# Performance work log

Hardware: AMD Instinct MI355X
Metric: run time of the kernel (lower is better)

## Reference

```python
import jax, jax.numpy as jnp
import numpy as np

B, N, D, H = 16, 1024, 768, 12
HD = D // H
SCALE = HD ** -0.5


def setup_inputs() -> dict:
    key = jax.random.key(0)
    ks = jax.random.split(key, 7)
    s = D ** -0.5
    return {
        "x": jax.random.normal(ks[0], (B, N, D), dtype=jnp.float32),
        "Wq": jax.random.normal(ks[1], (D, D), dtype=jnp.float32) * s,
        "bq": jax.random.normal(ks[2], (D,), dtype=jnp.float32) * 0.01,
        "Wk": jax.random.normal(ks[3], (D, D), dtype=jnp.float32) * s,
        "bk": jax.random.normal(ks[4], (D,), dtype=jnp.float32) * 0.01,
        "Wv": jax.random.normal(ks[5], (D, D), dtype=jnp.float32) * s,
        "bv": jax.random.normal(ks[6], (D,), dtype=jnp.float32) * 0.01,
    }


def _split_heads(t):
    # [B, N, D] -> [B, H, N, HD]
    return t.reshape(B, N, H, HD).transpose(0, 2, 1, 3)


def reference(x, Wq, bq, Wk, bk, Wv, bv):
    q = _split_heads(x @ Wq + bq)
    k = _split_heads(x @ Wk + bk)
    v = _split_heads(x @ Wv + bv)
    # [B, H, N, N] attention scores, fp32 softmax (matches eager path)
    scores = jnp.einsum("bhqd,bhkd->bhqk", q, k) * SCALE
    attn = jax.nn.softmax(scores.astype(jnp.float32), axis=-1).astype(q.dtype)
    # dropout p=0 in eval mode -> identity
    ctx = jnp.einsum("bhqk,bhkd->bhqd", attn, v)  # [B, H, N, HD]
    ctx = ctx.transpose(0, 2, 1, 3).reshape(B, N, D)
    return ctx
```

## Files before the change

kernel.cpp:

```cpp
#include <hip/hip_runtime.h>

#define B_ 16
#define N_ 1024
#define D_ 768
#define H_ 12
#define HD_ 64
#define QSCALE 0.18033688011112042f

typedef __attribute__((ext_vector_type(8))) __bf16 bf16x8;
typedef __attribute__((ext_vector_type(4))) float f32x4;
typedef unsigned short u16;
typedef unsigned int u32;

__device__ inline u16 f2bf(float f) {
    u32 u = __builtin_bit_cast(u32, f);
    u += 0x7fffu + ((u >> 16) & 1u);
    return (u16)(u >> 16);
}

__device__ inline float fexp2(float x) {
#if __has_builtin(__builtin_amdgcn_exp2f)
    return __builtin_amdgcn_exp2f(x);
#else
    return exp2f(x);
#endif
}

__device__ inline u32 cvt_pk_bf16(float a, float b) {
    u32 r;
    asm("v_cvt_pk_bf16_f32 %0, %1, %2" : "=v"(r) : "v"(a), "v"(b));
    return r;
}

__device__ inline void gl_lds16(const u16* gp, u16* lp_) {
    __builtin_amdgcn_global_load_lds(
        (const __attribute__((address_space(1))) u32*)(gp),
        (__attribute__((address_space(3))) u32*)(lp_), 16, 0, 0);
}

__global__ __launch_bounds__(256) void prep_kernel(
    const float* __restrict__ x, u16* __restrict__ xbf,
    const float* __restrict__ Wq, const float* __restrict__ Wk,
    const float* __restrict__ Wv, u16* __restrict__ wtall) {
    const int bid = blockIdx.x, tid = threadIdx.x;
    if (bid < 6144) {
        int i = bid * 256 + tid;
        const float4* p = (const float4*)x;
        float4 a = p[2 * i], b = p[2 * i + 1];
        union { u16 us[8]; int4 v; } u;
        u.us[0] = f2bf(a.x); u.us[1] = f2bf(a.y); u.us[2] = f2bf(a.z); u.us[3] = f2bf(a.w);
        u.us[4] = f2bf(b.x); u.us[5] = f2bf(b.y); u.us[6] = f2bf(b.z); u.us[7] = f2bf(b.w);
        ((int4*)xbf)[i] = u.v;
    } else {
        __shared__ u16 t[32][33];
        int wb = bid - 6144;
        int z = wb / 576, rem = wb % 576;
        int bx = rem % 24, by = rem / 24;
        const float* W = z == 0 ? Wq : (z == 1 ? Wk : Wv);
        u16* Wt = wtall + (size_t)z * D_ * D_;
        int n0 = bx * 32, k0 = by * 32;
        int tx = tid & 31, ty = tid >> 5;
#pragma unroll
        for (int i = 0; i < 4; i++) {
            int k = k0 + ty + i * 8;
            t[ty + i * 8][tx] = f2bf(W[k * D_ + n0 + tx]);
        }
        __syncthreads();
#pragma unroll
        for (int i = 0; i < 4; i++) {
            int n = n0 + ty + i * 8;
            Wt[n * D_ + k0 + tx] = t[tx][ty + i * 8];
        }
    }
}

__global__ __launch_bounds__(256) void qkv2_kernel(
    const u16* __restrict__ xbf, const u16* __restrict__ wtall,
    const float* __restrict__ bq, const float* __restrict__ bk, const float* __restrict__ bv,
    u16* __restrict__ qbf, u16* __restrict__ kbf, u16* __restrict__ vtbf) {
    __shared__ u16 lsA[2][128 * 64];
    __shared__ u16 lsB[2][128 * 64];

    const int mt = blockIdx.x, nt = blockIdx.y;
    const int tid = threadIdx.x, w = tid >> 6, lane = tid & 63;
    const int g = lane >> 4, c = lane & 15;
    const int wr = w >> 1, wc = w & 1;
    const int m0 = mt * 128, n0 = nt * 128;

    const u16* pa[4];
    const u16* pb[4];
#pragma unroll
    for (int i = 0; i < 4; i++) {
        int ch = (i * 4 + w) * 64 + lane;
        int row = ch >> 3, c8 = ch & 7;
        pa[i] = xbf + (size_t)(m0 + row) * D_ + c8 * 8;
        pb[i] = wtall + (size_t)(n0 + row) * D_ + c8 * 8;
    }

#define STAGE(bi, koff) do {                                       \
        _Pragma("unroll")                                          \
        for (int i = 0; i < 4; i++) {                              \
            gl_lds16(pa[i] + (koff), &lsA[bi][(i * 4 + w) * 512]); \
            gl_lds16(pb[i] + (koff), &lsB[bi][(i * 4 + w) * 512]); \
        }                                                          \
    } while (0)

    f32x4 acc[4][4];
#pragma unroll
    for (int i = 0; i < 4; i++)
#pragma unroll
        for (int j = 0; j < 4; j++) acc[i][j] = (f32x4){0.f, 0.f, 0.f, 0.f};

    STAGE(0, 0);
    __syncthreads();
    int cur = 0;

    for (int kt = 0; kt < 12; kt++) {
        if (kt < 11) STAGE(cur ^ 1, (kt + 1) * 64);
#pragma unroll
        for (int kk = 0; kk < 2; kk++) {
            bf16x8 af[4], bfr[4];
#pragma unroll
            for (int f = 0; f < 4; f++)
                af[f] = *(const bf16x8*)&lsA[cur][(wr * 64 + f * 16 + c) * 64 + kk * 32 + g * 8];
#pragma unroll
            for (int f = 0; f < 4; f++)
                bfr[f] = *(const bf16x8*)&lsB[cur][(wc * 64 + f * 16 + c) * 64 + kk * 32 + g * 8];
#pragma unroll
            for (int fr = 0; fr < 4; fr++)
#pragma unroll
                for (int fc = 0; fc < 4; fc++)
                    acc[fr][fc] = __builtin_amdgcn_mfma_f32_16x16x32_bf16(
                        af[fr], bfr[fc], acc[fr][fc], 0, 0, 0);
        }
        __syncthreads();
        cur ^= 1;
    }
#undef STAGE

    const int mode = nt / 6;
    const int ncol0 = (nt % 6) * 128;
    const float* bias = mode == 0 ? bq : (mode == 1 ? bk : bv);
    float bb[4];
#pragma unroll
    for (int fc = 0; fc < 4; fc++) bb[fc] = bias[ncol0 + wc * 64 + fc * 16 + c];

    if (mode < 2) {
        u16* outp = mode == 0 ? qbf : kbf;
        const float osc = mode == 0 ? QSCALE : 1.0f;
#pragma unroll
        for (int fc = 0; fc < 4; fc++) {
            int col = ncol0 + wc * 64 + fc * 16 + c;
            int head = col >> 6, hd = col & 63;
#pragma unroll
            for (int fr = 0; fr < 4; fr++)
#pragma unroll
                for (int rr = 0; rr < 4; rr++) {
                    int m = m0 + wr * 64 + fr * 16 + g * 4 + rr;
                    int b = m >> 10, nn = m & 1023;
                    outp[(((size_t)b * H_ + head) * N_ + nn) * HD_ + hd] =
                        f2bf((acc[fr][fc][rr] + bb[fc]) * osc);
                }
        }
    } else {
#pragma unroll
        for (int fc = 0; fc < 4; fc++) {
            int col = ncol0 + wc * 64 + fc * 16 + c;
            int head = col >> 6, hd = col & 63;
#pragma unroll
            for (int fr = 0; fr < 4; fr++) {
                int m = m0 + wr * 64 + fr * 16 + g * 4;
                int b = m >> 10, nn = m & 1023;
                union { u16 us[4]; int2 v; } u;
#pragma unroll
                for (int rr = 0; rr < 4; rr++) u.us[rr] = f2bf(acc[fr][fc][rr] + bb[fc]);
                *(int2*)&vtbf[(((size_t)b * H_ + head) * HD_ + hd) * N_ + nn] = u.v;
            }
        }
    }
}

__global__ __launch_bounds__(256) void attn_kernel(
    const u16* __restrict__ qbf, const u16* __restrict__ kbf,
    const u16* __restrict__ vtbf, float* __restrict__ out) {
    __shared__ u16 lk[2][64][72];
    __shared__ u16 lv[2][64][72];

    const int bh = blockIdx.x;
    const int qt = blockIdx.y;
    const int b = bh / H_, h = bh % H_;
    const int tid = threadIdx.x;
    const int w = tid >> 6, lane = tid & 63, g = lane >> 4, c = lane & 15;
    const int q0 = qt * 128;

    bf16x8 aq[2][2];
#pragma unroll
    for (int ss = 0; ss < 2; ss++) {
        const u16* qr = qbf + ((size_t)bh * N_ + q0 + w * 32 + ss * 16 + c) * HD_;
        aq[ss][0] = *(const bf16x8*)&qr[g * 8];
        aq[ss][1] = *(const bf16x8*)&qr[32 + g * 8];
    }

    const u16* kbase = kbf + (size_t)bh * N_ * HD_;
    const u16* vbase = vtbf + (size_t)bh * HD_ * N_;
    const int r0 = tid >> 3, c80 = (tid & 7) * 8;
    const int r1 = r0 + 32;

    int4 kreg0, kreg1, vreg0, vreg1;
#define LOADT(KV) do { \
        kreg0 = *(const int4*)(kbase + (size_t)((KV) + r0) * HD_ + c80); \
        kreg1 = *(const int4*)(kbase + (size_t)((KV) + r1) * HD_ + c80); \
        vreg0 = *(const int4*)(vbase + (size_t)r0 * N_ + (KV) + c80); \
        vreg1 = *(const int4*)(vbase + (size_t)r1 * N_ + (KV) + c80); \
    } while (0)
#define WRITET(bi) do { \
        *(int4*)&lk[bi][r0][c80] = kreg0; \
        *(int4*)&lk[bi][r1][c80] = kreg1; \
        *(int4*)&lv[bi][r0][c80] = vreg0; \
        *(int4*)&lv[bi][r1][c80] = vreg1; \
    } while (0)

    const f32x4 zf = (f32x4){0.f, 0.f, 0.f, 0.f};
    f32x4 o[2][4];
#pragma unroll
    for (int ss = 0; ss < 2; ss++)
#pragma unroll
        for (int i = 0; i < 4; i++) o[ss][i] = zf;
    float lr[2] = {0.f, 0.f};

    LOADT(0);
    WRITET(0);
    __syncthreads();
    int cur = 0;

    for (int kv0 = 0; kv0 < N_; kv0 += 64) {
        const bool more = (kv0 + 64) < N_;
        if (more) LOADT(kv0 + 64);

        f32x4 sc[2][4];
#pragma unroll
        for (int nf = 0; nf < 4; nf++) {
            bf16x8 ak0 = *(const bf16x8*)&lk[cur][nf * 16 + c][g * 8];
            bf16x8 ak1 = *(const bf16x8*)&lk[cur][nf * 16 + c][32 + g * 8];
            __builtin_amdgcn_s_setprio(1);
#pragma unroll
            for (int ss = 0; ss < 2; ss++) {
                sc[ss][nf] = __builtin_amdgcn_mfma_f32_16x16x32_bf16(ak0, aq[ss][0], zf, 0, 0, 0);
                sc[ss][nf] = __builtin_amdgcn_mfma_f32_16x16x32_bf16(ak1, aq[ss][1], sc[ss][nf], 0, 0, 0);
            }
            __builtin_amdgcn_s_setprio(0);
        }

        u32 pkk[2][4][2];
#pragma unroll
        for (int ss = 0; ss < 2; ss++) {
            f32x4 rsv = zf;
#pragma unroll
            for (int nf = 0; nf < 4; nf++) {
#pragma unroll
                for (int r = 0; r < 4; r++) sc[ss][nf][r] = fexp2(sc[ss][nf][r]);
                rsv += sc[ss][nf];
                pkk[ss][nf][0] = cvt_pk_bf16(sc[ss][nf][0], sc[ss][nf][1]);
                pkk[ss][nf][1] = cvt_pk_bf16(sc[ss][nf][2], sc[ss][nf][3]);
            }
            lr[ss] += (rsv[0] + rsv[1]) + (rsv[2] + rsv[3]);
        }

        bf16x8 pa[2][2];
#pragma unroll
        for (int ss = 0; ss < 2; ss++) {
            union { u32 ui[4]; bf16x8 v; } u0, u1;
            u0.ui[0] = pkk[ss][0][0]; u0.ui[1] = pkk[ss][0][1];
            u0.ui[2] = pkk[ss][1][0]; u0.ui[3] = pkk[ss][1][1];
            u1.ui[0] = pkk[ss][2][0]; u1.ui[1] = pkk[ss][2][1];
            u1.ui[2] = pkk[ss][3][0]; u1.ui[3] = pkk[ss][3][1];
            pa[ss][0] = u0.v; pa[ss][1] = u1.v;
        }

#pragma unroll
        for (int nf = 0; nf < 4; nf++) {
            union { int2 d[2]; bf16x8 v; } b0, b1;
            b0.d[0] = *(const int2*)&lv[cur][nf * 16 + c][4 * g];
            b0.d[1] = *(const int2*)&lv[cur][nf * 16 + c][16 + 4 * g];
            b1.d[0] = *(const int2*)&lv[cur][nf * 16 + c][32 + 4 * g];
            b1.d[1] = *(const int2*)&lv[cur][nf * 16 + c][48 + 4 * g];
            __builtin_amdgcn_s_setprio(1);
#pragma unroll
            for (int ss = 0; ss < 2; ss++) {
                o[ss][nf] = __builtin_amdgcn_mfma_f32_16x16x32_bf16(pa[ss][0], b0.v, o[ss][nf], 0, 0, 0);
                o[ss][nf] = __builtin_amdgcn_mfma_f32_16x16x32_bf16(pa[ss][1], b1.v, o[ss][nf], 0, 0, 0);
            }
            __builtin_amdgcn_s_setprio(0);
        }

        if (more) WRITET(cur ^ 1);
        __syncthreads();
        cur ^= 1;
    }
#undef LOADT
#undef WRITET

#pragma unroll
    for (int ss = 0; ss < 2; ss++) {
        float lf = lr[ss];
        lf += __shfl_xor(lf, 16);
        lf += __shfl_xor(lf, 32);
        float lq[4];
#pragma unroll
        for (int r = 0; r < 4; r++) lq[r] = __shfl(lf, g * 4 + r);
#pragma unroll
        for (int r = 0; r < 4; r++) {
            float inv = 1.f / lq[r];
            int n = q0 + w * 32 + ss * 16 + g * 4 + r;
#pragma unroll
            for (int nf = 0; nf < 4; nf++)
                out[((size_t)(b * N_ + n)) * D_ + h * HD_ + nf * 16 + c] = o[ss][nf][r] * inv;
        }
    }
}

extern "C" void kernel_launch(void* const* d_in, const int* in_sizes, int n_in,
                              void* d_out, int out_size, void* d_ws, size_t ws_size,
                              hipStream_t stream) {
    const float* x  = (const float*)d_in[0];
    const float* Wq = (const float*)d_in[1];
    const float* bq = (const float*)d_in[2];
    const float* Wk = (const float*)d_in[3];
    const float* bk = (const float*)d_in[4];
    const float* Wv = (const float*)d_in[5];
    const float* bv = (const float*)d_in[6];
    float* out = (float*)d_out;

    char* ws = (char*)d_ws;
    u16* xbf   = (u16*)ws;
    u16* wtall = (u16*)(ws + 25165824);
    u16* qbf   = (u16*)(ws + 28704768);
    u16* kbf   = (u16*)(ws + 53870592);
    u16* vtbf  = (u16*)(ws + 79036416);

    prep_kernel<<<7872, 256, 0, stream>>>(x, xbf, Wq, Wk, Wv, wtall);
    dim3 gg(128, 18);
    qkv2_kernel<<<gg, 256, 0, stream>>>(xbf, wtall, bq, bk, bv, qbf, kbf, vtbf);
    dim3 ga(192, 8);
    attn_kernel<<<ga, 256, 0, stream>>>(qbf, kbf, vtbf, out);
}
```

Baseline: 174.8 us.

## Pipeline QKV GEMM loads with 4-slot LDS ring and vmcnt waits

Restructures the QKV projection GEMM main loop from a double-buffered 64-wide K stage into a 4-slot ring of 32-wide K slices with two slices prefetched ahead. It replaces full __syncthreads with explicit s_waitcnt vmcnt counters plus a raw s_barrier, so global-to-LDS copies stay in flight across compute steps. The goal is to hide more global load latency behind MFMA work. LDS use stays the same. The risks are the hand-counted vmcnt values and the ring reuse: a barrier placed only before compute may leave a write-after-read hazard on a slot that is being refilled.

After: 175.5 us. No clear change (+0.4%).

```diff
diff --git a/kernel.cpp b/kernel.cpp
--- a/kernel.cpp
+++ b/kernel.cpp
@@ -78,8 +78,8 @@
     const u16* __restrict__ xbf, const u16* __restrict__ wtall,
     const float* __restrict__ bq, const float* __restrict__ bk, const float* __restrict__ bv,
     u16* __restrict__ qbf, u16* __restrict__ kbf, u16* __restrict__ vtbf) {
-    __shared__ u16 lsA[2][128 * 64];
-    __shared__ u16 lsB[2][128 * 64];
+    __shared__ u16 lsA[4 * 4096];
+    __shared__ u16 lsB[4 * 4096];
 
     const int mt = blockIdx.x, nt = blockIdx.y;
     const int tid = threadIdx.x, w = tid >> 6, lane = tid & 63;
@@ -87,22 +87,17 @@
     const int wr = w >> 1, wc = w & 1;
     const int m0 = mt * 128, n0 = nt * 128;
 
-    const u16* pa[4];
-    const u16* pb[4];
-#pragma unroll
-    for (int i = 0; i < 4; i++) {
-        int ch = (i * 4 + w) * 64 + lane;
-        int row = ch >> 3, c8 = ch & 7;
-        pa[i] = xbf + (size_t)(m0 + row) * D_ + c8 * 8;
-        pb[i] = wtall + (size_t)(n0 + row) * D_ + c8 * 8;
-    }
-
-#define STAGE(bi, koff) do {                                       \
-        _Pragma("unroll")                                          \
-        for (int i = 0; i < 4; i++) {                              \
-            gl_lds16(pa[i] + (koff), &lsA[bi][(i * 4 + w) * 512]); \
-            gl_lds16(pb[i] + (koff), &lsB[bi][(i * 4 + w) * 512]); \
-        }                                                          \
+    const int row0 = tid >> 2, cp0 = tid & 3;
+    const u16* ba0 = xbf + (size_t)(m0 + row0) * D_ + cp0 * 8;
+    const u16* ba1 = xbf + (size_t)(m0 + row0 + 64) * D_ + cp0 * 8;
+    const u16* bb0 = wtall + (size_t)(n0 + row0) * D_ + cp0 * 8;
+    const u16* bb1 = wtall + (size_t)(n0 + row0 + 64) * D_ + cp0 * 8;
+
+#define STAGEP(slot, p) do {                                   \
+        gl_lds16(ba0 + (p) * 32, &lsA[(slot) * 4096 + w * 512]);        \
+        gl_lds16(ba1 + (p) * 32, &lsA[(slot) * 4096 + 2048 + w * 512]); \
+        gl_lds16(bb0 + (p) * 32, &lsB[(slot) * 4096 + w * 512]);        \
+        gl_lds16(bb1 + (p) * 32, &lsB[(slot) * 4096 + 2048 + w * 512]); \
     } while (0)
 
     f32x4 acc[4][4];
@@ -111,32 +106,41 @@
 #pragma unroll
         for (int j = 0; j < 4; j++) acc[i][j] = (f32x4){0.f, 0.f, 0.f, 0.f};
 
-    STAGE(0, 0);
-    __syncthreads();
-    int cur = 0;
-
-    for (int kt = 0; kt < 12; kt++) {
-        if (kt < 11) STAGE(cur ^ 1, (kt + 1) * 64);
-#pragma unroll
-        for (int kk = 0; kk < 2; kk++) {
-            bf16x8 af[4], bfr[4];
-#pragma unroll
-            for (int f = 0; f < 4; f++)
-                af[f] = *(const bf16x8*)&lsA[cur][(wr * 64 + f * 16 + c) * 64 + kk * 32 + g * 8];
-#pragma unroll
-            for (int f = 0; f < 4; f++)
-                bfr[f] = *(const bf16x8*)&lsB[cur][(wc * 64 + f * 16 + c) * 64 + kk * 32 + g * 8];
-#pragma unroll
-            for (int fr = 0; fr < 4; fr++)
-#pragma unroll
-                for (int fc = 0; fc < 4; fc++)
-                    acc[fr][fc] = __builtin_amdgcn_mfma_f32_16x16x32_bf16(
-                        af[fr], bfr[fc], acc[fr][fc], 0, 0, 0);
-        }
-        __syncthreads();
-        cur ^= 1;
-    }
-#undef STAGE
+#define COMPUTE(s) do {                                                         \
+        bf16x8 af[4], bfr[4];                                                   \
+        _Pragma("unroll")                                                       \
+        for (int f = 0; f < 4; f++)                                             \
+            af[f] = *(const bf16x8*)&lsA[(s) * 4096 + (wr * 64 + f * 16 + c) * 32 + g * 8]; \
+        _Pragma("unroll")                                                       \
+        for (int f = 0; f < 4; f++)                                             \
+            bfr[f] = *(const bf16x8*)&lsB[(s) * 4096 + (wc * 64 + f * 16 + c) * 32 + g * 8]; \
+        _Pragma("unroll")                                                       \
+        for (int fr = 0; fr < 4; fr++)                                          \
+            _Pragma("unroll")                                                   \
+            for (int fc = 0; fc < 4; fc++)                                      \
+                acc[fr][fc] = __builtin_amdgcn_mfma_f32_16x16x32_bf16(          \
+                    af[fr], bfr[fc], acc[fr][fc], 0, 0, 0);                     \
+    } while (0)
+
+    STAGEP(0, 0);
+    STAGEP(1, 1);
+    for (int p = 0; p < 22; ++p) {
+        STAGEP((p + 2) & 3, p + 2);
+        asm volatile("s_waitcnt vmcnt(8)" ::: "memory");
+        __builtin_amdgcn_s_barrier();
+        __builtin_amdgcn_sched_barrier(0);
+        COMPUTE(p & 3);
+    }
+    asm volatile("s_waitcnt vmcnt(4)" ::: "memory");
+    __builtin_amdgcn_s_barrier();
+    __builtin_amdgcn_sched_barrier(0);
+    COMPUTE(2);
+    asm volatile("s_waitcnt vmcnt(0)" ::: "memory");
+    __builtin_amdgcn_s_barrier();
+    __builtin_amdgcn_sched_barrier(0);
+    COMPUTE(3);
+#undef STAGEP
+#undef COMPUTE
 
     const int mode = nt / 6;
     const int ncol0 = (nt % 6) * 128;
```
